# Optimization experiments

Measured on AMD Instinct MI355X. Metric: run time of the kernel, lower is better.

The kernel has to match this reference:

```python
import jax, jax.numpy as jnp
import numpy as np

N, D, H = 1024, 128, 512
EPS = 1e-5  # torch LayerNorm default


def setup_inputs() -> dict:
    key = jax.random.key(0)
    ks = jax.random.split(key, 8)
    emb = jax.random.normal(ks[0], (N, D), dtype=jnp.float32)
    emb = emb / jnp.linalg.norm(emb, axis=-1, keepdims=True)  # L2-normalised GAT embeddings
    s1 = 1.0 / np.sqrt(2 * D)
    s2 = 1.0 / np.sqrt(H)
    s3 = 1.0 / np.sqrt(H // 2)
    return {
        "embeddings": emb,
        "W1": jax.random.uniform(ks[1], (2 * D, H), jnp.float32, -s1, s1),
        "b1": jnp.zeros((H,), jnp.float32),
        "gamma": jnp.ones((H,), jnp.float32),
        "beta": jnp.zeros((H,), jnp.float32),
        "W2": jax.random.uniform(ks[2], (H, H // 2), jnp.float32, -s2, s2),
        "b2": jnp.zeros((H // 2,), jnp.float32),
        "W3": jax.random.uniform(ks[3], (H // 2, 1), jnp.float32, -s3, s3),
        "b3": jnp.zeros((1,), jnp.float32),
    }


def reference(embeddings, W1, b1, gamma, beta, W2, b2, W3, b3):
    n = embeddings.shape[0]
    idx_i, idx_j = jnp.triu_indices(n, k=1)          # E = n(n-1)/2
    pairs = jnp.stack([idx_i, idx_j], axis=1)        # [E, 2]
    e_i = embeddings[idx_i]                          # [E, D]
    e_j = embeddings[idx_j]
    feats = jnp.concatenate([e_i - e_j, e_i * e_j], axis=-1)  # [E, 2D]
    h = jax.nn.relu(feats @ W1 + b1)                 # [E, H]
    mu = jnp.mean(h, axis=-1, keepdims=True)
    var = jnp.mean(jnp.square(h - mu), axis=-1, keepdims=True)
    h = (h - mu) * jax.lax.rsqrt(var + EPS) * gamma + beta
    # dropout is identity at inference
    h = jax.nn.relu(h @ W2 + b2)                     # [E, H//2]
    logits = (h @ W3 + b3)[:, 0]                     # [E]
    return logits, pairs
```

## Files before the change

### kernel.cpp

```cpp
#include <hip/hip_runtime.h>

typedef __attribute__((ext_vector_type(8))) int i32x8;
typedef __attribute__((ext_vector_type(16))) float f32x16;
typedef unsigned int u32;
typedef unsigned char u8;

#define NN 1024
#define ETOT 523776
#define EPSV 1e-5f

#define L_PSUM 0
#define L_PSQ  3072
#define L_B1   6144
#define L_G    8192
#define L_BB   9216
#define L_W3   10240
#define L_TILE 11264
#define L_TOTAL 44032

#define SCL1 0x7F7F7F7F

__device__ __forceinline__ u32 pk4fp8(float a, float b, float c, float d) {
  int p = __builtin_amdgcn_cvt_pk_fp8_f32(a, b, 0, false);
  p = __builtin_amdgcn_cvt_pk_fp8_f32(c, d, p, true);
  return (u32)p;
}
__device__ __forceinline__ i32x8 ldg32(const u8* p) {
  uint4 lo = *(const uint4*)p;
  uint4 hi = *(const uint4*)(p + 16);
  i32x8 r;
  r[0]=(int)lo.x; r[1]=(int)lo.y; r[2]=(int)lo.z; r[3]=(int)lo.w;
  r[4]=(int)hi.x; r[5]=(int)hi.y; r[6]=(int)hi.z; r[7]=(int)hi.w;
  return r;
}
__device__ __forceinline__ i32x8 lds32(const char* base, int e8) {
  uint2 s0 = *(const uint2*)(base + e8);
  uint2 s1 = *(const uint2*)(base + 512 + e8);
  uint2 s2 = *(const uint2*)(base + 1024 + e8);
  uint2 s3 = *(const uint2*)(base + 1536 + e8);
  i32x8 r;
  r[0]=(int)s0.x; r[1]=(int)s0.y; r[2]=(int)s1.x; r[3]=(int)s1.y;
  r[4]=(int)s2.x; r[5]=(int)s2.y; r[6]=(int)s3.x; r[7]=(int)s3.y;
  return r;
}
#define MFMA64(A,B,C) __builtin_amdgcn_mfma_scale_f32_32x32x64_f8f6f4((A),(B),(C),0,0,0,SCL1,0,SCL1)

__global__ void prep_w(const float* __restrict__ W1, const float* __restrict__ W2,
                       const float* __restrict__ gammav,
                       u8* __restrict__ W1f, u8* __restrict__ W2f) {
  int idx = blockIdx.x*256 + threadIdx.x;
  { int c = idx >> 8, k = idx & 255;
    float v = W1[k*512 + c] * 64.f;
    int p = __builtin_amdgcn_cvt_pk_fp8_f32(v, 0.f, 0, false);
    W1f[(c>>5)*8192 + (k>>6)*2048 + ((k>>5)&1)*1024 + (c&31)*32 + (k&31)] = (u8)(p & 0xff); }
  { int o = idx >> 9, c = idx & 511;
    float v = gammav[c] * W2[c*256 + o] * 64.f;
    int p = __builtin_amdgcn_cvt_pk_fp8_f32(v, 0.f, 0, false);
    W2f[(o>>5)*16384 + (c>>6)*2048 + ((c>>5)&1)*1024 + (o&31)*32 + (c&31)] = (u8)(p & 0xff); }
}

__global__ void prep_vec(const float* __restrict__ W2, const float* __restrict__ gammav,
                         const float* __restrict__ betav, const float* __restrict__ b2v,
                         float* __restrict__ Gv, float* __restrict__ BBv) {
  int o = blockIdx.x, t = threadIdx.x;
  float g = 0.f, bb = 0.f;
  for (int c = t; c < 512; c += 64) {
    float w = W2[c*256 + o];
    g  += gammav[c] * w;
    bb += betav[c]  * w;
  }
  #pragma unroll
  for (int off = 1; off < 64; off <<= 1) {
    g  += __shfl_xor(g,  off, 64);
    bb += __shfl_xor(bb, off, 64);
  }
  if (t == 0) { Gv[o] = g; BBv[o] = bb + b2v[o]; }
}

__launch_bounds__(512, 4)
__global__ void edge_main(const float* __restrict__ emb,
                          const float* __restrict__ b1v,
                          const float* __restrict__ b3v,
                          const float* __restrict__ w3v,
                          const float* __restrict__ Gv,
                          const float* __restrict__ BBv,
                          const u8* __restrict__ W1f,
                          const u8* __restrict__ W2f,
                          float* __restrict__ out) {
  extern __shared__ char smem[];
  float* psum = (float*)(smem + L_PSUM);
  float* psq  = (float*)(smem + L_PSQ);
  float* sb1  = (float*)(smem + L_B1);
  float* sG   = (float*)(smem + L_G);
  float* sBB  = (float*)(smem + L_BB);
  float* sw3  = (float*)(smem + L_W3);
  char*  tile = smem + L_TILE;
  char*  A1   = tile + 16384;

  const int tid  = threadIdx.x;
  const int w    = tid >> 6;
  const int lane = tid & 63;
  const int l31  = lane & 31;
  const int hi   = lane >> 5;

  int kblk = blockIdx.x;
  int bi = (int)((257.0f - sqrtf(66049.0f - 8.0f*(float)kblk)) * 0.5f);
  bi = bi < 0 ? 0 : (bi > 127 ? 127 : bi);
  while (bi*128 - bi*(bi-1)/2 > kblk) --bi;
  while ((bi+1)*128 - (bi+1)*bi/2 <= kblk) ++bi;
  const int bj = bi + (kblk - (bi*128 - bi*(bi-1)/2));
  const int i0 = bi*8, j0 = bj*8;

  {
    const int e  = lane;
    const int d0 = (w & 3) * 32;
    const float4* pei = (const float4*)(emb + (i0 + (e>>3))*128 + d0);
    const float4* pej = (const float4*)(emb + (j0 + (e&7))*128 + d0);
    char* base = A1 + (w>>1)*4096 + (w&1)*2048 + e*8;
    #pragma unroll
    for (int s = 0; s < 4; ++s) {
      float4 x0 = pei[s*2], x1 = pei[s*2+1];
      float4 y0 = pej[s*2], y1 = pej[s*2+1];
      uint2 pk;
      if (w < 4) {
        pk.x = pk4fp8((x0.x-y0.x)*4.f, (x0.y-y0.y)*4.f, (x0.z-y0.z)*4.f, (x0.w-y0.w)*4.f);
        pk.y = pk4fp8((x1.x-y1.x)*4.f, (x1.y-y1.y)*4.f, (x1.z-y1.z)*4.f, (x1.w-y1.w)*4.f);
      } else {
        pk.x = pk4fp8((x0.x*y0.x)*4.f, (x0.y*y0.y)*4.f, (x0.z*y0.z)*4.f, (x0.w*y0.w)*4.f);
        pk.y = pk4fp8((x1.x*y1.x)*4.f, (x1.y*y1.y)*4.f, (x1.z*y1.z)*4.f, (x1.w*y1.w)*4.f);
      }
      *(uint2*)(base + s*512) = pk;
    }
  }
  sb1[tid] = b1v[tid] * 16.f;
  if (tid < 256) { sG[tid] = Gv[tid]; sBB[tid] = BBv[tid]; sw3[tid] = w3v[tid]; }
  __syncthreads();

  f32x16 z16;
  #pragma unroll
  for (int i = 0; i < 16; ++i) z16[i] = 0.f;

  float sumS0 = 0.f, sqS0 = 0.f, sumS1 = 0.f, sqS1 = 0.f;
  f32x16 A0, A1acc;

  auto h1pass = [&](int cb, const f32x16& E0, const f32x16& E1) {
    char* dbase = tile + (cb>>1)*4096 + (cb&1)*2048 + hi*4;
    #pragma unroll
    for (int g = 0; g < 4; ++g) {
      const int c0 = cb*32 + g*8 + hi*4;
      const float b0 = sb1[c0+0], b1_ = sb1[c0+1], b2_ = sb1[c0+2], b3_ = sb1[c0+3];
      char* dst = dbase + g*512;
      {
        float v0 = fmaxf(fmaf(E0[g*4+0], 0.0625f, b0), 0.f);
        float v1 = fmaxf(fmaf(E0[g*4+1], 0.0625f, b1_), 0.f);
        float v2 = fmaxf(fmaf(E0[g*4+2], 0.0625f, b2_), 0.f);
        float v3 = fmaxf(fmaf(E0[g*4+3], 0.0625f, b3_), 0.f);
        *(u32*)(dst + l31*8) = pk4fp8(v0, v1, v2, v3);
        sumS0 += (v0+v1)+(v2+v3);
        sqS0 = fmaf(v0,v0,sqS0); sqS0 = fmaf(v1,v1,sqS0);
        sqS0 = fmaf(v2,v2,sqS0); sqS0 = fmaf(v3,v3,sqS0);
      }
      {
        float v0 = fmaxf(fmaf(E1[g*4+0], 0.0625f, b0), 0.f);
        float v1 = fmaxf(fmaf(E1[g*4+1], 0.0625f, b1_), 0.f);
        float v2 = fmaxf(fmaf(E1[g*4+2], 0.0625f, b2_), 0.f);
        float v3 = fmaxf(fmaf(E1[g*4+3], 0.0625f, b3_), 0.f);
        *(u32*)(dst + (l31+32)*8) = pk4fp8(v0, v1, v2, v3);
        sumS1 += (v0+v1)+(v2+v3);
        sqS1 = fmaf(v0,v0,sqS1); sqS1 = fmaf(v1,v1,sqS1);
        sqS1 = fmaf(v2,v2,sqS1); sqS1 = fmaf(v3,v3,sqS1);
      }
    }
  };

  const u8* w1base = W1f + hi*1024 + l31*32;

  A0 = z16; A1acc = z16;
  #pragma unroll
  for (int kq = 0; kq < 4; ++kq) {
    i32x8 af = ldg32(w1base + w*8192 + kq*2048);
    const char* bbp = A1 + kq*4096 + hi*2048;
    i32x8 bf0 = lds32(bbp, l31*8);
    i32x8 bf1 = lds32(bbp, (l31+32)*8);
    A0    = MFMA64(af, bf0, A0);
    A1acc = MFMA64(af, bf1, A1acc);
  }
  h1pass(w, A0, A1acc);

  A0 = z16; A1acc = z16;
  #pragma unroll
  for (int kq = 0; kq < 4; ++kq) {
    i32x8 af = ldg32(w1base + (w+8)*8192 + kq*2048);
    const char* bbp = A1 + kq*4096 + hi*2048;
    i32x8 bf0 = lds32(bbp, l31*8);
    i32x8 bf1 = lds32(bbp, (l31+32)*8);
    A0    = MFMA64(af, bf0, A0);
    A1acc = MFMA64(af, bf1, A1acc);
  }
  __syncthreads();
  h1pass(w + 8, A0, A1acc);

  sumS0 += __shfl_xor(sumS0, 32, 64);  sqS0 += __shfl_xor(sqS0, 32, 64);
  sumS1 += __shfl_xor(sumS1, 32, 64);  sqS1 += __shfl_xor(sqS1, 32, 64);
  if (hi == 0) {
    psum[l31*12 + w] = sumS0;       psq[l31*12 + w] = sqS0;
    psum[(l31+32)*12 + w] = sumS1;  psq[(l31+32)*12 + w] = sqS1;
  }
  __syncthreads();

  float sc2A, smA, sc2B, smB;
  {
    float4 s0 = *(const float4*)(psum + l31*12);
    float4 s1 = *(const float4*)(psum + l31*12 + 4);
    float4 q0 = *(const float4*)(psq  + l31*12);
    float4 q1 = *(const float4*)(psq  + l31*12 + 4);
    float su = ((s0.x+s0.y)+(s0.z+s0.w)) + ((s1.x+s1.y)+(s1.z+s1.w));
    float qu = ((q0.x+q0.y)+(q0.z+q0.w)) + ((q1.x+q1.y)+(q1.z+q1.w));
    float mu = su * (1.f/8192.f);
    float sc = rsqrtf(qu * (1.f/131072.f) - mu*mu + EPSV);
    sc2A = sc * (1.f/1024.f); smA = mu * sc;
    s0 = *(const float4*)(psum + (l31+32)*12);
    s1 = *(const float4*)(psum + (l31+32)*12 + 4);
    q0 = *(const float4*)(psq  + (l31+32)*12);
    q1 = *(const float4*)(psq  + (l31+32)*12 + 4);
    su = ((s0.x+s0.y)+(s0.z+s0.w)) + ((s1.x+s1.y)+(s1.z+s1.w));
    qu = ((q0.x+q0.y)+(q0.z+q0.w)) + ((q1.x+q1.y)+(q1.z+q1.w));
    mu = su * (1.f/8192.f);
    sc = rsqrtf(qu * (1.f/131072.f) - mu*mu + EPSV);
    sc2B = sc * (1.f/1024.f); smB = mu * sc;
  }

  f32x16 C0 = z16, C1 = z16;
  {
    const u8* w2base = W2f + w*16384 + hi*1024 + l31*32;
    #pragma unroll
    for (int kq = 0; kq < 8; ++kq) {
      i32x8 a = ldg32(w2base + kq*2048);
      const char* bbp = tile + kq*4096 + hi*2048;
      i32x8 b0 = lds32(bbp, l31*8);
      i32x8 b1 = lds32(bbp, (l31+32)*8);
      C0 = MFMA64(a, b0, C0);
      C1 = MFMA64(a, b1, C1);
    }
  }

  {
    float p0 = 0.f, p1 = 0.f;
    #pragma unroll
    for (int rg = 0; rg < 16; ++rg) {
      const int o = w*32 + (rg&3) + 8*(rg>>2) + 4*hi;
      const float gv = sG[o], bb = sBB[o], w3 = sw3[o];
      float t0 = fmaxf(fmaf(sc2A, C0[rg], fmaf(-smA, gv, bb)), 0.f);
      p0 = fmaf(t0, w3, p0);
      float t1 = fmaxf(fmaf(sc2B, C1[rg], fmaf(-smB, gv, bb)), 0.f);
      p1 = fmaf(t1, w3, p1);
    }
    p0 += __shfl_xor(p0, 32, 64);
    p1 += __shfl_xor(p1, 32, 64);
    if (hi == 0) {
      sb1[l31*8 + w] = p0;
      sb1[(l31+32)*8 + w] = p1;
    }
  }
  __syncthreads();

  if (tid < 64) {
    float4 s0 = *(const float4*)(sb1 + tid*8);
    float4 s1 = *(const float4*)(sb1 + tid*8 + 4);
    float logit = ((s0.x+s0.y)+(s0.z+s0.w)) + ((s1.x+s1.y)+(s1.z+s1.w)) + b3v[0];
    int a = tid >> 3, b = tid & 7;
    int i = i0 + a, j = j0 + b;
    if (i < j) {
      int e = i*(2*NN - i - 1)/2 + (j - i - 1);
      out[e] = logit;
      out[ETOT + 2*e]     = (float)i;
      out[ETOT + 2*e + 1] = (float)j;
    }
  }
}

extern "C" void kernel_launch(void* const* d_in, const int* in_sizes, int n_in,
                              void* d_out, int out_size, void* d_ws, size_t ws_size,
                              hipStream_t stream) {
  const float* emb   = (const float*)d_in[0];
  const float* W1    = (const float*)d_in[1];
  const float* b1    = (const float*)d_in[2];
  const float* gamma = (const float*)d_in[3];
  const float* beta  = (const float*)d_in[4];
  const float* W2    = (const float*)d_in[5];
  const float* b2    = (const float*)d_in[6];
  const float* W3    = (const float*)d_in[7];
  const float* b3    = (const float*)d_in[8];

  char* ws   = (char*)d_ws;
  u8*  W1f = (u8*)ws;
  u8*  W2f = (u8*)(ws + 131072);
  float* Gv  = (float*)(ws + 262144);
  float* BBv = (float*)(ws + 263168);

  (void)hipFuncSetAttribute((const void*)edge_main,
                            hipFuncAttributeMaxDynamicSharedMemorySize, L_TOTAL);

  prep_w<<<512, 256, 0, stream>>>(W1, W2, gamma, W1f, W2f);
  prep_vec<<<256, 64, 0, stream>>>(W2, gamma, beta, b2, Gv, BBv);
  edge_main<<<8256, 512, L_TOTAL, stream>>>(emb, b1, b3, W3, Gv, BBv,
                                            W1f, W2f, (float*)d_out);
}
```

Baseline: 204.8 us.

## Shrink edge tiles to 8x4 pairs with 256-thread blocks and wider LDS fragment loads

Each block now handles 32 edges (8x4 node tile) with 4 waves instead of 64 edges with 8 waves, doubling the block count and halving shared memory per block. Each wave now computes two output column tiles against one shared B fragment, so every weight fragment loaded from global memory feeds a single MFMA on 32 edges instead of two. B-fragment loads from LDS become two 16-byte reads instead of four 8-byte reads. The intent is higher occupancy and better load balance with cheaper LDS access, at the cost of twice as much total weight traffic per edge and more block launches.

```diff
diff --git a/kernel.cpp b/kernel.cpp
--- a/kernel.cpp
+++ b/kernel.cpp
@@ -8,15 +8,17 @@
 #define NN 1024
 #define ETOT 523776
 #define EPSV 1e-5f
+#define NBLK 16512
 
 #define L_PSUM 0
-#define L_PSQ  3072
-#define L_B1   6144
-#define L_G    8192
-#define L_BB   9216
-#define L_W3   10240
-#define L_TILE 11264
-#define L_TOTAL 44032
+#define L_PSQ  512
+#define L_EP   1024
+#define L_B1   1536
+#define L_G    3584
+#define L_BB   4608
+#define L_W3   5632
+#define L_TILE 6656
+#define L_TOTAL 23040
 
 #define SCL1 0x7F7F7F7F
 
@@ -25,23 +27,15 @@
   p = __builtin_amdgcn_cvt_pk_fp8_f32(c, d, p, true);
   return (u32)p;
 }
-__device__ __forceinline__ i32x8 ldg32(const u8* p) {
-  uint4 lo = *(const uint4*)p;
-  uint4 hi = *(const uint4*)(p + 16);
-  i32x8 r;
-  r[0]=(int)lo.x; r[1]=(int)lo.y; r[2]=(int)lo.z; r[3]=(int)lo.w;
-  r[4]=(int)hi.x; r[5]=(int)hi.y; r[6]=(int)hi.z; r[7]=(int)hi.w;
-  return r;
-}
-__device__ __forceinline__ i32x8 lds32(const char* base, int e8) {
-  uint2 s0 = *(const uint2*)(base + e8);
-  uint2 s1 = *(const uint2*)(base + 512 + e8);
-  uint2 s2 = *(const uint2*)(base + 1024 + e8);
-  uint2 s3 = *(const uint2*)(base + 1536 + e8);
-  i32x8 r;
-  r[0]=(int)s0.x; r[1]=(int)s0.y; r[2]=(int)s1.x; r[3]=(int)s1.y;
-  r[4]=(int)s2.x; r[5]=(int)s2.y; r[6]=(int)s3.x; r[7]=(int)s3.y;
-  return r;
+
+struct u4x2 { uint4 a, b; };
+__device__ __forceinline__ i32x8 fragg(const u8* p) {
+  u4x2 t; t.a = *(const uint4*)p; t.b = *(const uint4*)(p + 16);
+  return __builtin_bit_cast(i32x8, t);
+}
+__device__ __forceinline__ i32x8 fragl(const char* p) {
+  u4x2 t; t.a = *(const uint4*)p; t.b = *(const uint4*)(p + 512);
+  return __builtin_bit_cast(i32x8, t);
 }
 #define MFMA64(A,B,C) __builtin_amdgcn_mfma_scale_f32_32x32x64_f8f6f4((A),(B),(C),0,0,0,SCL1,0,SCL1)
 
@@ -77,7 +71,7 @@
   if (t == 0) { Gv[o] = g; BBv[o] = bb + b2v[o]; }
 }
 
-__launch_bounds__(512, 4)
+__launch_bounds__(256, 5)
 __global__ void edge_main(const float* __restrict__ emb,
                           const float* __restrict__ b1v,
                           const float* __restrict__ b3v,
@@ -90,12 +84,13 @@
   extern __shared__ char smem[];
   float* psum = (float*)(smem + L_PSUM);
   float* psq  = (float*)(smem + L_PSQ);
+  float* epart= (float*)(smem + L_EP);
   float* sb1  = (float*)(smem + L_B1);
   float* sG   = (float*)(smem + L_G);
   float* sBB  = (float*)(smem + L_BB);
   float* sw3  = (float*)(smem + L_W3);
   char*  tile = smem + L_TILE;
-  char*  A1   = tile + 16384;
+  char*  A1p  = tile + 8192;
 
   const int tid  = threadIdx.x;
   const int w    = tid >> 6;
@@ -104,172 +99,146 @@
   const int hi   = lane >> 5;
 
   int kblk = blockIdx.x;
-  int bi = (int)((257.0f - sqrtf(66049.0f - 8.0f*(float)kblk)) * 0.5f);
+  int bi = (int)((257.0f - sqrtf(66049.0f - 4.0f*(float)kblk)) * 0.5f);
   bi = bi < 0 ? 0 : (bi > 127 ? 127 : bi);
-  while (bi*128 - bi*(bi-1)/2 > kblk) --bi;
-  while ((bi+1)*128 - (bi+1)*bi/2 <= kblk) ++bi;
-  const int bj = bi + (kblk - (bi*128 - bi*(bi-1)/2));
-  const int i0 = bi*8, j0 = bj*8;
-
-  {
-    const int e  = lane;
-    const int d0 = (w & 3) * 32;
-    const float4* pei = (const float4*)(emb + (i0 + (e>>3))*128 + d0);
-    const float4* pej = (const float4*)(emb + (j0 + (e&7))*128 + d0);
-    char* base = A1 + (w>>1)*4096 + (w&1)*2048 + e*8;
-    #pragma unroll
-    for (int s = 0; s < 4; ++s) {
-      float4 x0 = pei[s*2], x1 = pei[s*2+1];
-      float4 y0 = pej[s*2], y1 = pej[s*2+1];
-      uint2 pk;
-      if (w < 4) {
-        pk.x = pk4fp8((x0.x-y0.x)*4.f, (x0.y-y0.y)*4.f, (x0.z-y0.z)*4.f, (x0.w-y0.w)*4.f);
-        pk.y = pk4fp8((x1.x-y1.x)*4.f, (x1.y-y1.y)*4.f, (x1.z-y1.z)*4.f, (x1.w-y1.w)*4.f);
-      } else {
-        pk.x = pk4fp8((x0.x*y0.x)*4.f, (x0.y*y0.y)*4.f, (x0.z*y0.z)*4.f, (x0.w*y0.w)*4.f);
-        pk.y = pk4fp8((x1.x*y1.x)*4.f, (x1.y*y1.y)*4.f, (x1.z*y1.z)*4.f, (x1.w*y1.w)*4.f);
+  while (bi > 0 && bi*(257 - bi) > kblk) --bi;
+  while ((bi+1)*(256 - bi) <= kblk) ++bi;
+  const int bj = 2*bi + (kblk - bi*(257 - bi));
+  const int i0 = bi*8, j0 = bj*4;
+
+  {
+    const int a = l31 >> 2, b = l31 & 3;
+    const int d0 = (w & 1)*64 + hi*32;
+    const float4* pei = (const float4*)(emb + (i0 + a)*128 + d0);
+    const float4* pej = (const float4*)(emb + (j0 + b)*128 + d0);
+    char* base = A1p + w*2048 + hi*1024 + l31*16;
+    #pragma unroll
+    for (int p = 0; p < 2; ++p) {
+      uint4 v;
+      u32* vp = (u32*)&v;
+      #pragma unroll
+      for (int s = 0; s < 4; ++s) {
+        float4 x = pei[p*4 + s];
+        float4 y = pej[p*4 + s];
+        vp[s] = (w < 2)
+          ? pk4fp8((x.x-y.x)*4.f, (x.y-y.y)*4.f, (x.z-y.z)*4.f, (x.w-y.w)*4.f)
+          : pk4fp8((x.x*y.x)*4.f, (x.y*y.y)*4.f, (x.z*y.z)*4.f, (x.w*y.w)*4.f);
       }
-      *(uint2*)(base + s*512) = pk;
+      *(uint4*)(base + p*512) = v;
     }
   }
   sb1[tid] = b1v[tid] * 16.f;
-  if (tid < 256) { sG[tid] = Gv[tid]; sBB[tid] = BBv[tid]; sw3[tid] = w3v[tid]; }
+  sb1[tid + 256] = b1v[tid + 256] * 16.f;
+  sG[tid] = Gv[tid]; sBB[tid] = BBv[tid]; sw3[tid] = w3v[tid];
   __syncthreads();
 
   f32x16 z16;
   #pragma unroll
   for (int i = 0; i < 16; ++i) z16[i] = 0.f;
 
-  float sumS0 = 0.f, sqS0 = 0.f, sumS1 = 0.f, sqS1 = 0.f;
-  f32x16 A0, A1acc;
-
-  auto h1pass = [&](int cb, const f32x16& E0, const f32x16& E1) {
-    char* dbase = tile + (cb>>1)*4096 + (cb&1)*2048 + hi*4;
+  float sumS = 0.f, sqS = 0.f;
+
+  auto h1pass = [&](int cb, const f32x16& E) {
+    char* dbase = tile + (cb>>1)*2048 + ((cb&1)<<1)*512 + l31*16 + hi*4;
     #pragma unroll
     for (int g = 0; g < 4; ++g) {
       const int c0 = cb*32 + g*8 + hi*4;
       const float b0 = sb1[c0+0], b1_ = sb1[c0+1], b2_ = sb1[c0+2], b3_ = sb1[c0+3];
-      char* dst = dbase + g*512;
-      {
-        float v0 = fmaxf(fmaf(E0[g*4+0], 0.0625f, b0), 0.f);
-        float v1 = fmaxf(fmaf(E0[g*4+1], 0.0625f, b1_), 0.f);
-        float v2 = fmaxf(fmaf(E0[g*4+2], 0.0625f, b2_), 0.f);
-        float v3 = fmaxf(fmaf(E0[g*4+3], 0.0625f, b3_), 0.f);
-        *(u32*)(dst + l31*8) = pk4fp8(v0, v1, v2, v3);
-        sumS0 += (v0+v1)+(v2+v3);
-        sqS0 = fmaf(v0,v0,sqS0); sqS0 = fmaf(v1,v1,sqS0);
-        sqS0 = fmaf(v2,v2,sqS0); sqS0 = fmaf(v3,v3,sqS0);
-      }
-      {
-        float v0 = fmaxf(fmaf(E1[g*4+0], 0.0625f, b0), 0.f);
-        float v1 = fmaxf(fmaf(E1[g*4+1], 0.0625f, b1_), 0.f);
-        float v2 = fmaxf(fmaf(E1[g*4+2], 0.0625f, b2_), 0.f);
-        float v3 = fmaxf(fmaf(E1[g*4+3], 0.0625f, b3_), 0.f);
-        *(u32*)(dst + (l31+32)*8) = pk4fp8(v0, v1, v2, v3);
-        sumS1 += (v0+v1)+(v2+v3);
-        sqS1 = fmaf(v0,v0,sqS1); sqS1 = fmaf(v1,v1,sqS1);
-        sqS1 = fmaf(v2,v2,sqS1); sqS1 = fmaf(v3,v3,sqS1);
-      }
+      float v0 = fmaxf(fmaf(E[g*4+0], 0.0625f, b0), 0.f);
+      float v1 = fmaxf(fmaf(E[g*4+1], 0.0625f, b1_), 0.f);
+      float v2 = fmaxf(fmaf(E[g*4+2], 0.0625f, b2_), 0.f);
+      float v3 = fmaxf(fmaf(E[g*4+3], 0.0625f, b3_), 0.f);
+      *(u32*)(dbase + (g>>1)*512 + (g&1)*8) = pk4fp8(v0, v1, v2, v3);
+      sumS += (v0+v1)+(v2+v3);
+      sqS = fmaf(v0,v0,sqS); sqS = fmaf(v1,v1,sqS);
+      sqS = fmaf(v2,v2,sqS); sqS = fmaf(v3,v3,sqS);
     }
   };
 
-  const u8* w1base = W1f + hi*1024 + l31*32;
-
-  A0 = z16; A1acc = z16;
-  #pragma unroll
-  for (int kq = 0; kq < 4; ++kq) {
-    i32x8 af = ldg32(w1base + w*8192 + kq*2048);
-    const char* bbp = A1 + kq*4096 + hi*2048;
-    i32x8 bf0 = lds32(bbp, l31*8);
-    i32x8 bf1 = lds32(bbp, (l31+32)*8);
-    A0    = MFMA64(af, bf0, A0);
-    A1acc = MFMA64(af, bf1, A1acc);
-  }
-  h1pass(w, A0, A1acc);
-
-  A0 = z16; A1acc = z16;
-  #pragma unroll
-  for (int kq = 0; kq < 4; ++kq) {
-    i32x8 af = ldg32(w1base + (w+8)*8192 + kq*2048);
-    const char* bbp = A1 + kq*4096 + hi*2048;
-    i32x8 bf0 = lds32(bbp, l31*8);
-    i32x8 bf1 = lds32(bbp, (l31+32)*8);
-    A0    = MFMA64(af, bf0, A0);
-    A1acc = MFMA64(af, bf1, A1acc);
-  }
+  const u8*  w1b = W1f + hi*1024 + l31*32;
+  const char* a1r = A1p + hi*1024 + l31*16;
+
+  {
+    f32x16 acc0 = z16, acc1 = z16;
+    #pragma unroll
+    for (int kq = 0; kq < 4; ++kq) {
+      i32x8 af0 = fragg(w1b + (w  )*8192 + kq*2048);
+      i32x8 af1 = fragg(w1b + (w+4)*8192 + kq*2048);
+      i32x8 bf  = fragl(a1r + kq*2048);
+      acc0 = MFMA64(af0, bf, acc0);
+      acc1 = MFMA64(af1, bf, acc1);
+    }
+    h1pass(w,     acc0);
+    h1pass(w + 4, acc1);
+  }
+
+  {
+    f32x16 acc0 = z16, acc1 = z16;
+    #pragma unroll
+    for (int kq = 0; kq < 4; ++kq) {
+      i32x8 af0 = fragg(w1b + (w+ 8)*8192 + kq*2048);
+      i32x8 af1 = fragg(w1b + (w+12)*8192 + kq*2048);
+      i32x8 bf  = fragl(a1r + kq*2048);
+      acc0 = MFMA64(af0, bf, acc0);
+      acc1 = MFMA64(af1, bf, acc1);
+    }
+    __syncthreads();
+    h1pass(w + 8,  acc0);
+    h1pass(w + 12, acc1);
+  }
+
+  sumS += __shfl_xor(sumS, 32, 64);
+  sqS  += __shfl_xor(sqS,  32, 64);
+  if (hi == 0) { psum[l31*4 + w] = sumS; psq[l31*4 + w] = sqS; }
   __syncthreads();
-  h1pass(w + 8, A0, A1acc);
-
-  sumS0 += __shfl_xor(sumS0, 32, 64);  sqS0 += __shfl_xor(sqS0, 32, 64);
-  sumS1 += __shfl_xor(sumS1, 32, 64);  sqS1 += __shfl_xor(sqS1, 32, 64);
-  if (hi == 0) {
-    psum[l31*12 + w] = sumS0;       psq[l31*12 + w] = sqS0;
-    psum[(l31+32)*12 + w] = sumS1;  psq[(l31+32)*12 + w] = sqS1;
-  }
-  __syncthreads();
-
-  float sc2A, smA, sc2B, smB;
-  {
-    float4 s0 = *(const float4*)(psum + l31*12);
-    float4 s1 = *(const float4*)(psum + l31*12 + 4);
-    float4 q0 = *(const float4*)(psq  + l31*12);
-    float4 q1 = *(const float4*)(psq  + l31*12 + 4);
-    float su = ((s0.x+s0.y)+(s0.z+s0.w)) + ((s1.x+s1.y)+(s1.z+s1.w));
-    float qu = ((q0.x+q0.y)+(q0.z+q0.w)) + ((q1.x+q1.y)+(q1.z+q1.w));
+
+  float sc2A, smA;
+  {
+    float4 s = *(const float4*)(psum + l31*4);
+    float4 q = *(const float4*)(psq  + l31*4);
+    float su = (s.x+s.y)+(s.z+s.w);
+    float qu = (q.x+q.y)+(q.z+q.w);
     float mu = su * (1.f/8192.f);
     float sc = rsqrtf(qu * (1.f/131072.f) - mu*mu + EPSV);
-    sc2A = sc * (1.f/1024.f); smA = mu * sc;
-    s0 = *(const float4*)(psum + (l31+32)*12);
-    s1 = *(const float4*)(psum + (l31+32)*12 + 4);
-    q0 = *(const float4*)(psq  + (l31+32)*12);
-    q1 = *(const float4*)(psq  + (l31+32)*12 + 4);
-    su = ((s0.x+s0.y)+(s0.z+s0.w)) + ((s1.x+s1.y)+(s1.z+s1.w));
-    qu = ((q0.x+q0.y)+(q0.z+q0.w)) + ((q1.x+q1.y)+(q1.z+q1.w));
-    mu = su * (1.f/8192.f);
-    sc = rsqrtf(qu * (1.f/131072.f) - mu*mu + EPSV);
-    sc2B = sc * (1.f/1024.f); smB = mu * sc;
+    sc2A = sc * (1.f/1024.f);
+    smA  = mu * sc;
   }
 
   f32x16 C0 = z16, C1 = z16;
   {
-    const u8* w2base = W2f + w*16384 + hi*1024 + l31*32;
+    const u8* w2b = W2f + hi*1024 + l31*32;
+    const char* hrp = tile + hi*1024 + l31*16;
     #pragma unroll
     for (int kq = 0; kq < 8; ++kq) {
-      i32x8 a = ldg32(w2base + kq*2048);
-      const char* bbp = tile + kq*4096 + hi*2048;
-      i32x8 b0 = lds32(bbp, l31*8);
-      i32x8 b1 = lds32(bbp, (l31+32)*8);
-      C0 = MFMA64(a, b0, C0);
-      C1 = MFMA64(a, b1, C1);
-    }
-  }
-
-  {
-    float p0 = 0.f, p1 = 0.f;
+      i32x8 a0 = fragg(w2b + (2*w  )*16384 + kq*2048);
+      i32x8 a1 = fragg(w2b + (2*w+1)*16384 + kq*2048);
+      i32x8 b  = fragl(hrp + kq*2048);
+      C0 = MFMA64(a0, b, C0);
+      C1 = MFMA64(a1, b, C1);
+    }
+  }
+
+  {
+    float p = 0.f;
     #pragma unroll
     for (int rg = 0; rg < 16; ++rg) {
-      const int o = w*32 + (rg&3) + 8*(rg>>2) + 4*hi;
-      const float gv = sG[o], bb = sBB[o], w3 = sw3[o];
-      float t0 = fmaxf(fmaf(sc2A, C0[rg], fmaf(-smA, gv, bb)), 0.f);
-      p0 = fmaf(t0, w3, p0);
-      float t1 = fmaxf(fmaf(sc2B, C1[rg], fmaf(-smB, gv, bb)), 0.f);
-      p1 = fmaf(t1, w3, p1);
-    }
-    p0 += __shfl_xor(p0, 32, 64);
-    p1 += __shfl_xor(p1, 32, 64);
-    if (hi == 0) {
-      sb1[l31*8 + w] = p0;
-      sb1[(l31+32)*8 + w] = p1;
-    }
+      const int oo = (rg&3) + 8*(rg>>2) + 4*hi;
+      { const int o = (2*w)*32 + oo;
+        float t = fmaxf(fmaf(sc2A, C0[rg], fmaf(-smA, sG[o], sBB[o])), 0.f);
+        p = fmaf(t, sw3[o], p); }
+      { const int o = (2*w+1)*32 + oo;
+        float t = fmaxf(fmaf(sc2A, C1[rg], fmaf(-smA, sG[o], sBB[o])), 0.f);
+        p = fmaf(t, sw3[o], p); }
+    }
+    p += __shfl_xor(p, 32, 64);
+    if (hi == 0) epart[l31*4 + w] = p;
   }
   __syncthreads();
 
-  if (tid < 64) {
-    float4 s0 = *(const float4*)(sb1 + tid*8);
-    float4 s1 = *(const float4*)(sb1 + tid*8 + 4);
-    float logit = ((s0.x+s0.y)+(s0.z+s0.w)) + ((s1.x+s1.y)+(s1.z+s1.w)) + b3v[0];
-    int a = tid >> 3, b = tid & 7;
-    int i = i0 + a, j = j0 + b;
+  if (tid < 32) {
+    float4 s = *(const float4*)(epart + tid*4);
+    float logit = (s.x+s.y)+(s.z+s.w) + b3v[0];
+    int i = i0 + (tid >> 2), j = j0 + (tid & 3);
     if (i < j) {
       int e = i*(2*NN - i - 1)/2 + (j - i - 1);
       out[e] = logit;
@@ -298,11 +267,8 @@
   float* Gv  = (float*)(ws + 262144);
   float* BBv = (float*)(ws + 263168);
 
-  (void)hipFuncSetAttribute((const void*)edge_main,
-                            hipFuncAttributeMaxDynamicSharedMemorySize, L_TOTAL);
-
   prep_w<<<512, 256, 0, stream>>>(W1, W2, gamma, W1f, W2f);
   prep_vec<<<256, 64, 0, stream>>>(W2, gamma, beta, b2, Gv, BBv);
-  edge_main<<<8256, 512, L_TOTAL, stream>>>(emb, b1, b3, W3, Gv, BBv,
+  edge_main<<<NBLK, 256, L_TOTAL, stream>>>(emb, b1, b3, W3, Gv, BBv,
                                             W1f, W2f, (float*)d_out);
 }
```

Result: slower. 236.8 us (+15.7%).
